# Kernel tuning notes

Measured on AMD Instinct MI355X. Metric: run time of the kernel, lower is better.

Reference implementation:

```python
import jax, jax.numpy as jnp
import numpy as np

N = 50000      # num nodes
E = 800000     # num edges
F_IN = 128     # CONFIG.FeatureLen()
H = 100        # conv1_hide
C = 16         # CONFIG.ClassNum()
LEAKY = 0.01


def setup_inputs() -> dict:
    key = jax.random.key(0)
    k = jax.random.split(key, 4)
    x = jax.random.normal(k[0], (N, F_IN), dtype=jnp.float32)
    edge_index = jax.random.randint(k[1], (2, E), 0, N, dtype=jnp.int32)
    W1 = jax.random.normal(k[2], (F_IN, H), dtype=jnp.float32) / np.sqrt(F_IN).astype(np.float32)
    b1 = jnp.zeros((H,), dtype=jnp.float32)
    W2 = jax.random.normal(k[3], (H, C), dtype=jnp.float32) / np.sqrt(H).astype(np.float32)
    b2 = jnp.zeros((C,), dtype=jnp.float32)
    return {"x": x, "W1": W1, "b1": b1, "W2": W2, "b2": b2, "edge_index": edge_index}


def _gcn_conv(x, W, b, src, dst):
    """PyG GCNConv: x' = D^{-1/2}(A+I)D^{-1/2} X W + b (symmetric norm, self-loops)."""
    x = x @ W  # transform first (smaller feature dim for propagation)
    loop = jnp.arange(N, dtype=src.dtype)
    s = jnp.concatenate([src, loop])  # sources (message senders)
    d = jnp.concatenate([dst, loop])  # targets (message receivers)
    deg = jax.ops.segment_sum(jnp.ones_like(d, dtype=x.dtype), d, num_segments=N)
    dinv = jnp.where(deg > 0, jax.lax.rsqrt(deg), 0.0)
    norm = dinv[s] * dinv[d]                      # [E+N]
    msg = x[s] * norm[:, None]                    # gather + scale
    out = jax.ops.segment_sum(msg, d, num_segments=N)  # scatter-add
    return out + b


def reference(x, W1, b1, W2, b2, edge_index):
    src, dst = edge_index[0], edge_index[1]
    h = _gcn_conv(x, W1, b1, src, dst)
    h = jax.nn.leaky_relu(h, negative_slope=LEAKY)
    # dropout is identity in eval mode (training=False)
    h = _gcn_conv(h, W2, b2, src, dst)
    return jax.nn.log_softmax(h, axis=1)
```

## Files before the change

### kernel.cpp

```cpp
#include <hip/hip_runtime.h>

#define F_IN 128
#define HDIM 100
#define HPAD 128
#define CDIM 16
#define CAP  64
#define BT_STRIDE 136
#define CHUNK 4096
#define KMAX 200
#define RCAP 64

static constexpr float LEAKY = 0.01f;

using short8  = __attribute__((ext_vector_type(8))) short;
using float4v = __attribute__((ext_vector_type(4))) float;
using float2v = __attribute__((ext_vector_type(2))) float;

__device__ __forceinline__ unsigned short f2bf(float f) {
    unsigned u = __float_as_uint(f);
    u += 0x7fffu + ((u >> 16) & 1u);
    return (unsigned short)(u >> 16);
}


__global__ __launch_bounds__(256) void k_gemm1_p1(const float* __restrict__ x,
                                                  const float* __restrict__ W1,
                                                  unsigned char* __restrict__ y1f8,
                                                  const int* __restrict__ src,
                                                  const int* __restrict__ dst,
                                                  unsigned* __restrict__ bkt_edges,
                                                  int* __restrict__ cnt_arr,
                                                  int N, int E, int FB, int KBKT, int GB) {
    __shared__ union {
        unsigned short bt[F_IN * BT_STRIDE];
        struct { unsigned stage[CHUNK]; int cnt[KMAX]; } p1;
    } sm;
    int bx = blockIdx.x;
    int t = threadIdx.x;

    if (bx < FB) {
        unsigned* stage = sm.p1.stage;
        int* cnt = sm.p1.cnt;
        for (int i = t; i < KBKT; i += 256) cnt[i] = 0;
        __syncthreads();
        int e0 = bx * CHUNK, e1 = min(E, e0 + CHUNK);
        for (int i = e0 + t; i < e1; i += 256) {
            int d = dst[i];
            unsigned pk = ((unsigned)d << 16) | (unsigned)src[i];
            atomicAdd(&cnt[d >> 8], 1);
            stage[i - e0] = pk;
        }
        __syncthreads();
        for (int i = t; i < KBKT; i += 256) cnt_arr[bx * KBKT + i] = cnt[i];
        __syncthreads();
        for (int i = t; i < KBKT; i += 256) cnt[i] = 0;
        __syncthreads();
        int m = e1 - e0;
        for (int i = t; i < m; i += 256) {
            unsigned pk = stage[i];
            int b = pk >> 24;
            int pos = atomicAdd(&cnt[b], 1);
            if (pos < RCAP)
                bkt_edges[((size_t)b * FB + bx) * RCAP + pos] = pk;
        }
        return;
    }

    for (int idx = t; idx < F_IN * HPAD; idx += 256) {
        int k = idx >> 7;
        int n = idx & 127;
        float v = (n < HDIM) ? W1[k * HDIM + n] : 0.f;
        sm.bt[n * BT_STRIDE + k] = f2bf(v);
    }
    __syncthreads();

    int wave = t >> 6, lane = t & 63;
    int Mtiles = (N + 15) >> 4;
    int m = lane & 15;
    int kq = lane >> 4;

    for (int tile = (bx - FB) * 4 + wave; tile < Mtiles; tile += 4 * GB) {
        int row0 = tile * 16;
        int arow = min(row0 + m, N - 1);
        const float* xrow = x + (size_t)arow * F_IN;

        short8 afrag[4];
        #pragma unroll
        for (int kt = 0; kt < 4; ++kt) {
            int kb = kt * 32 + kq * 8;
            float4 a0 = *(const float4*)(xrow + kb);
            float4 a1 = *(const float4*)(xrow + kb + 4);
            short8 f;
            f[0] = (short)f2bf(a0.x); f[1] = (short)f2bf(a0.y);
            f[2] = (short)f2bf(a0.z); f[3] = (short)f2bf(a0.w);
            f[4] = (short)f2bf(a1.x); f[5] = (short)f2bf(a1.y);
            f[6] = (short)f2bf(a1.z); f[7] = (short)f2bf(a1.w);
            afrag[kt] = f;
        }

        bool full = (row0 + 15 < N);
        #pragma unroll
        for (int ct = 0; ct < 8; ++ct) {
            float4v acc = {0.f, 0.f, 0.f, 0.f};
            #pragma unroll
            for (int kt = 0; kt < 4; ++kt) {
                short8 b = *(const short8*)&sm.bt[(ct * 16 + m) * BT_STRIDE + kt * 32 + kq * 8];
                acc = __builtin_amdgcn_mfma_f32_16x16x32_bf16(afrag[kt], b, acc, 0, 0, 0);
            }
            #pragma unroll
            for (int i = 0; i < 4; ++i) {
                int r = row0 + kq * 4 + i;
                int v8 = __builtin_amdgcn_cvt_pk_fp8_f32(acc[i], acc[i], 0, false);
                if (full || r < N)
                    y1f8[(size_t)r * HPAD + ct * 16 + m] = (unsigned char)(v8 & 0xff);
            }
        }
    }
}


__global__ __launch_bounds__(256) void k_p2(const unsigned* __restrict__ bkt_edges,
                                            const int* __restrict__ cnt_arr,
                                            int* __restrict__ deg,
                                            unsigned short* __restrict__ slots,
                                            int N, int FB, int KBKT) {
    __shared__ int cur[256];
    int b = blockIdx.x, t = threadIdx.x;
    cur[t] = 0;
    __syncthreads();
    for (int fb = t; fb < FB; fb += 256) {
        int c = cnt_arr[fb * KBKT + b];
        size_t base = ((size_t)b * FB + fb) * RCAP;
        for (int j = 0; j < c; ++j) {
            unsigned pk = bkt_edges[base + j];
            int d = pk >> 16;
            int pos = atomicAdd(&cur[d & 255], 1);
            if (pos < CAP)
                slots[(size_t)d * CAP + pos] = (unsigned short)(pk & 0xffffu);
        }
    }
    __syncthreads();
    int n = (b << 8) + t;
    if (n < N) deg[n] = cur[t];
}


__global__ __launch_bounds__(256) void k_agg1y2(const unsigned* __restrict__ y1u,
                                                const float* __restrict__ b1,
                                                const float* __restrict__ W2,
                                                const int* __restrict__ deg,
                                                const unsigned short* __restrict__ slots,
                                                float* __restrict__ y2, int N) {
    __shared__ float W2s[HDIM * CDIM];
    __shared__ float hs[4][2][HPAD];
    int t = threadIdx.x;
    for (int idx = t; idx < HDIM * CDIM; idx += 256) W2s[idx] = W2[idx];
    __syncthreads();

    int wave = t >> 6, lane = t & 63;
    int half = lane >> 5, l = lane & 31;
    int hbase = lane & 32;
    int n = blockIdx.x * 8 + wave * 2 + half;
    bool valid = (n < N);
    int nn = valid ? n : (N - 1);

    int beg = nn * CAP;
    int cnt = valid ? deg[nn] : 0;
    float dn = rsqrtf((float)deg[nn] + 1.0f);

    int cother = __shfl(cnt, lane ^ 32);
    int cmax = max(cnt, cother);

    float a0 = 0.f, a1 = 0.f, a2 = 0.f, a3 = 0.f;
    for (int e0 = 0; e0 < cmax; e0 += 32) {
        int mm = min(32, cnt - e0);
        unsigned su = 0u; float wv = 0.f;
        if (l < mm) {
            su = slots[beg + e0 + l];
            wv = rsqrtf((float)deg[su] + 1.0f);
        }
        int mmax = min(32, cmax - e0);
        int mpad = (mmax + 7) & ~7;
        for (int j = 0; j < mpad; j += 8) {
            float w[8]; unsigned vv[8];
            #pragma unroll
            for (int q = 0; q < 8; ++q) {
                int ln = hbase | (j + q);
                unsigned s = (unsigned)__shfl((int)su, ln);
                w[q] = __shfl(wv, ln);
                vv[q] = y1u[(size_t)s * 32 + l];
            }
            #pragma unroll
            for (int q = 0; q < 8; ++q) {
                float2v lov = __builtin_amdgcn_cvt_pk_f32_fp8((int)vv[q], false);
                float2v hiv = __builtin_amdgcn_cvt_pk_f32_fp8((int)vv[q], true);
                a0 = fmaf(w[q], lov[0], a0);
                a1 = fmaf(w[q], lov[1], a1);
                a2 = fmaf(w[q], hiv[0], a2);
                a3 = fmaf(w[q], hiv[1], a3);
            }
        }
    }
    {
        unsigned vn = y1u[(size_t)nn * 32 + l];
        float2v lov = __builtin_amdgcn_cvt_pk_f32_fp8((int)vn, false);
        float2v hiv = __builtin_amdgcn_cvt_pk_f32_fp8((int)vn, true);
        a0 = fmaf(dn, lov[0], a0);
        a1 = fmaf(dn, lov[1], a1);
        a2 = fmaf(dn, hiv[0], a2);
        a3 = fmaf(dn, hiv[1], a3);
    }

    float4 bb = (l < 25) ? *(const float4*)&b1[4 * l] : make_float4(0.f, 0.f, 0.f, 0.f);
    float h0 = fmaf(dn, a0, bb.x);
    float h1 = fmaf(dn, a1, bb.y);
    float h2 = fmaf(dn, a2, bb.z);
    float h3 = fmaf(dn, a3, bb.w);
    h0 = h0 > 0.f ? h0 : LEAKY * h0;
    h1 = h1 > 0.f ? h1 : LEAKY * h1;
    h2 = h2 > 0.f ? h2 : LEAKY * h2;
    h3 = h3 > 0.f ? h3 : LEAKY * h3;
    *(float4*)&hs[wave][half][4 * l] = make_float4(h0, h1, h2, h3);
    __builtin_amdgcn_wave_barrier();

    int c = l & 15, kg = l >> 4;
    const float* hrow = hs[wave][half];
    float p = 0.f;
    #pragma unroll 10
    for (int j = 0; j < 50; ++j) {
        int k = 2 * j + kg;
        p = fmaf(hrow[k], W2s[k * CDIM + c], p);
    }
    p += __shfl_down(p, 16);
    if (l < 16 && valid) y2[(size_t)n * CDIM + c] = p;
}


__global__ __launch_bounds__(256) void k_agg2(const float* __restrict__ y2,
                                              const float* __restrict__ b2,
                                              const int* __restrict__ deg,
                                              const unsigned short* __restrict__ slots,
                                              float* __restrict__ out, int N) {
    int t = threadIdx.x;
    int wave = t >> 6, lane = t & 63;
    int sub = lane >> 4, c = lane & 15;
    int n = blockIdx.x * 16 + wave * 4 + sub;
    bool valid = (n < N);
    int nn = valid ? n : 0;

    int beg = nn * CAP;
    int cnt = valid ? deg[nn] : 0;
    float dn = rsqrtf((float)deg[nn] + 1.0f);
    float acc = dn * y2[(size_t)nn * CDIM + c];

    for (int e0 = 0; e0 < cnt; e0 += 16) {
        int mm = min(16, cnt - e0);
        unsigned su = 0u; float wv = 0.f;
        if (c < mm) {
            su = slots[beg + e0 + c];
            wv = rsqrtf((float)deg[su] + 1.0f);
        }
        int mpad = (mm + 3) & ~3;
        for (int j = 0; j < mpad; j += 4) {
            float w[4]; float v[4];
            #pragma unroll
            for (int q = 0; q < 4; ++q) {
                int ln = sub * 16 + j + q;
                unsigned s = (unsigned)__shfl((int)su, ln);
                w[q] = __shfl(wv, ln);
                v[q] = y2[(size_t)s * CDIM + c];
            }
            #pragma unroll
            for (int q = 0; q < 4; ++q) acc = fmaf(w[q], v[q], acc);
        }
    }

    float lg = fmaf(dn, acc, b2[c]);
    float mx = lg;
    #pragma unroll
    for (int k = 8; k; k >>= 1) mx = fmaxf(mx, __shfl_xor(mx, k));
    float ex = __expf(lg - mx);
    #pragma unroll
    for (int k = 8; k; k >>= 1) ex += __shfl_xor(ex, k);
    float lse = mx + __logf(ex);
    if (valid) out[(size_t)n * CDIM + c] = lg - lse;
}


extern "C" void kernel_launch(void* const* d_in, const int* in_sizes, int n_in,
                              void* d_out, int out_size, void* d_ws, size_t ws_size,
                              hipStream_t stream) {
    const float* x  = (const float*)d_in[0];
    const float* W1 = (const float*)d_in[1];
    const float* b1 = (const float*)d_in[2];
    const float* W2 = (const float*)d_in[3];
    const float* b2 = (const float*)d_in[4];
    const int*   ei = (const int*)d_in[5];

    const int N = in_sizes[0] / F_IN;
    const int E = in_sizes[5] / 2;
    const int* src = ei;
    const int* dst = ei + E;

    const int KBKT = (N + 255) >> 8;
    const int FB   = (E + CHUNK - 1) / CHUNK;

    char* ws = (char*)d_ws;
    size_t off = 0;
    auto alloc = [&](size_t bytes) {
        char* p = ws + off;
        off += (bytes + 255) & ~(size_t)255;
        return p;
    };
    int*            deg       = (int*)alloc((size_t)N * 4);
    unsigned char*  y1f8      = (unsigned char*)alloc((size_t)N * HPAD);
    float*          y2        = (float*)alloc((size_t)N * CDIM * 4);
    unsigned short* slots     = (unsigned short*)alloc((size_t)N * CAP * 2);
    int*            cnt_arr   = (int*)alloc((size_t)FB * KBKT * 4);
    unsigned*       bkt_edges = (unsigned*)alloc((size_t)KBKT * FB * RCAP * 4);
    (void)ws_size; (void)n_in; (void)out_size;

    const int GB = 262;

    k_gemm1_p1<<<FB + GB, 256, 0, stream>>>(x, W1, y1f8, src, dst,
                                            bkt_edges, cnt_arr, N, E, FB, KBKT, GB);
    k_p2<<<KBKT, 256, 0, stream>>>(bkt_edges, cnt_arr, deg, slots, N, FB, KBKT);
    k_agg1y2<<<(N + 7) / 8, 256, 0, stream>>>((const unsigned*)y1f8, b1, W2,
                                              deg, slots, y2, N);
    k_agg2<<<(N + 15) / 16, 256, 0, stream>>>(y2, b2, deg, slots,
                                              (float*)d_out, N);
}
```

Before: 163.3 us.

## Replace two-pass bucketed CSR build with direct global atomic scatter

Removes the block-local bucketing pass and the separate k_p2 kernel. Edges are now scattered straight into per-node slot lists using global atomicAdd on deg, after a memset. This drops the intermediate bucket buffers and one kernel launch, but relies on many scattered global atomics and makes slot order nondeterministic.

```diff
diff --git a/kernel.cpp b/kernel.cpp
--- a/kernel.cpp
+++ b/kernel.cpp
@@ -6,9 +6,6 @@
 #define CDIM 16
 #define CAP  64
 #define BT_STRIDE 136
-#define CHUNK 4096
-#define KMAX 200
-#define RCAP 64
 
 static constexpr float LEAKY = 0.01f;
 
@@ -23,45 +20,26 @@
 }
 
 
-__global__ __launch_bounds__(256) void k_gemm1_p1(const float* __restrict__ x,
-                                                  const float* __restrict__ W1,
-                                                  unsigned char* __restrict__ y1f8,
-                                                  const int* __restrict__ src,
-                                                  const int* __restrict__ dst,
-                                                  unsigned* __restrict__ bkt_edges,
-                                                  int* __restrict__ cnt_arr,
-                                                  int N, int E, int FB, int KBKT, int GB) {
-    __shared__ union {
-        unsigned short bt[F_IN * BT_STRIDE];
-        struct { unsigned stage[CHUNK]; int cnt[KMAX]; } p1;
-    } sm;
+__global__ __launch_bounds__(256) void k_gemm1_scat(const float* __restrict__ x,
+                                                    const float* __restrict__ W1,
+                                                    unsigned char* __restrict__ y1f8,
+                                                    const int* __restrict__ src,
+                                                    const int* __restrict__ dst,
+                                                    int* __restrict__ deg,
+                                                    unsigned short* __restrict__ slots,
+                                                    int N, int E, int GB, int SC) {
+    __shared__ unsigned short bt[F_IN * BT_STRIDE];
     int bx = blockIdx.x;
     int t = threadIdx.x;
 
-    if (bx < FB) {
-        unsigned* stage = sm.p1.stage;
-        int* cnt = sm.p1.cnt;
-        for (int i = t; i < KBKT; i += 256) cnt[i] = 0;
-        __syncthreads();
-        int e0 = bx * CHUNK, e1 = min(E, e0 + CHUNK);
-        for (int i = e0 + t; i < e1; i += 256) {
+    if (bx >= GB) {
+        int stride = SC * 256;
+        for (int i = (bx - GB) * 256 + t; i < E; i += stride) {
             int d = dst[i];
-            unsigned pk = ((unsigned)d << 16) | (unsigned)src[i];
-            atomicAdd(&cnt[d >> 8], 1);
-            stage[i - e0] = pk;
-        }
-        __syncthreads();
-        for (int i = t; i < KBKT; i += 256) cnt_arr[bx * KBKT + i] = cnt[i];
-        __syncthreads();
-        for (int i = t; i < KBKT; i += 256) cnt[i] = 0;
-        __syncthreads();
-        int m = e1 - e0;
-        for (int i = t; i < m; i += 256) {
-            unsigned pk = stage[i];
-            int b = pk >> 24;
-            int pos = atomicAdd(&cnt[b], 1);
-            if (pos < RCAP)
-                bkt_edges[((size_t)b * FB + bx) * RCAP + pos] = pk;
+            int s = src[i];
+            int pos = atomicAdd(&deg[d], 1);
+            if (pos < CAP)
+                slots[(size_t)d * CAP + pos] = (unsigned short)s;
         }
         return;
     }
@@ -70,7 +48,7 @@
         int k = idx >> 7;
         int n = idx & 127;
         float v = (n < HDIM) ? W1[k * HDIM + n] : 0.f;
-        sm.bt[n * BT_STRIDE + k] = f2bf(v);
+        bt[n * BT_STRIDE + k] = f2bf(v);
     }
     __syncthreads();
 
@@ -79,7 +57,7 @@
     int m = lane & 15;
     int kq = lane >> 4;
 
-    for (int tile = (bx - FB) * 4 + wave; tile < Mtiles; tile += 4 * GB) {
+    for (int tile = bx * 4 + wave; tile < Mtiles; tile += 4 * GB) {
         int row0 = tile * 16;
         int arow = min(row0 + m, N - 1);
         const float* xrow = x + (size_t)arow * F_IN;
@@ -104,7 +82,7 @@
             float4v acc = {0.f, 0.f, 0.f, 0.f};
             #pragma unroll
             for (int kt = 0; kt < 4; ++kt) {
-                short8 b = *(const short8*)&sm.bt[(ct * 16 + m) * BT_STRIDE + kt * 32 + kq * 8];
+                short8 b = *(const short8*)&bt[(ct * 16 + m) * BT_STRIDE + kt * 32 + kq * 8];
                 acc = __builtin_amdgcn_mfma_f32_16x16x32_bf16(afrag[kt], b, acc, 0, 0, 0);
             }
             #pragma unroll
@@ -116,32 +94,6 @@
             }
         }
     }
-}
-
-
-__global__ __launch_bounds__(256) void k_p2(const unsigned* __restrict__ bkt_edges,
-                                            const int* __restrict__ cnt_arr,
-                                            int* __restrict__ deg,
-                                            unsigned short* __restrict__ slots,
-                                            int N, int FB, int KBKT) {
-    __shared__ int cur[256];
-    int b = blockIdx.x, t = threadIdx.x;
-    cur[t] = 0;
-    __syncthreads();
-    for (int fb = t; fb < FB; fb += 256) {
-        int c = cnt_arr[fb * KBKT + b];
-        size_t base = ((size_t)b * FB + fb) * RCAP;
-        for (int j = 0; j < c; ++j) {
-            unsigned pk = bkt_edges[base + j];
-            int d = pk >> 16;
-            int pos = atomicAdd(&cur[d & 255], 1);
-            if (pos < CAP)
-                slots[(size_t)d * CAP + pos] = (unsigned short)(pk & 0xffffu);
-        }
-    }
-    __syncthreads();
-    int n = (b << 8) + t;
-    if (n < N) deg[n] = cur[t];
 }
 
 
@@ -302,9 +254,6 @@
     const int* src = ei;
     const int* dst = ei + E;
 
-    const int KBKT = (N + 255) >> 8;
-    const int FB   = (E + CHUNK - 1) / CHUNK;
-
     char* ws = (char*)d_ws;
     size_t off = 0;
     auto alloc = [&](size_t bytes) {
@@ -312,19 +261,18 @@
         off += (bytes + 255) & ~(size_t)255;
         return p;
     };
-    int*            deg       = (int*)alloc((size_t)N * 4);
-    unsigned char*  y1f8      = (unsigned char*)alloc((size_t)N * HPAD);
-    float*          y2        = (float*)alloc((size_t)N * CDIM * 4);
-    unsigned short* slots     = (unsigned short*)alloc((size_t)N * CAP * 2);
-    int*            cnt_arr   = (int*)alloc((size_t)FB * KBKT * 4);
-    unsigned*       bkt_edges = (unsigned*)alloc((size_t)KBKT * FB * RCAP * 4);
+    int*            deg   = (int*)alloc((size_t)N * 4);
+    unsigned char*  y1f8  = (unsigned char*)alloc((size_t)N * HPAD);
+    float*          y2    = (float*)alloc((size_t)N * CDIM * 4);
+    unsigned short* slots = (unsigned short*)alloc((size_t)N * CAP * 2);
     (void)ws_size; (void)n_in; (void)out_size;
 
     const int GB = 262;
-
-    k_gemm1_p1<<<FB + GB, 256, 0, stream>>>(x, W1, y1f8, src, dst,
-                                            bkt_edges, cnt_arr, N, E, FB, KBKT, GB);
-    k_p2<<<KBKT, 256, 0, stream>>>(bkt_edges, cnt_arr, deg, slots, N, FB, KBKT);
+    const int SC = 512;
+
+    hipMemsetAsync(deg, 0, (size_t)N * 4, stream);
+    k_gemm1_scat<<<GB + SC, 256, 0, stream>>>(x, W1, y1f8, src, dst,
+                                              deg, slots, N, E, GB, SC);
     k_agg1y2<<<(N + 7) / 8, 256, 0, stream>>>((const unsigned*)y1f8, b1, W2,
                                               deg, slots, y2, N);
     k_agg2<<<(N + 15) / 16, 256, 0, stream>>>(y2, b2, deg, slots,
```

Result: slower. 171.5 us (+5.1%).

## Replace layer-2 pull aggregation with atomic edge push and precomputed dinv

Applied to the files above, without the earlier changes.

Degree normalisation factors are computed once in the bucketing kernel and stored, so the aggregation kernels no longer recompute rsqrt per neighbour. The second-layer aggregation becomes two kernels. The first pushes pre-scaled y2 rows along the raw edge list with float atomics into an accumulator seeded with the self-loop term, and a separate kernel applies the destination scale, the bias and log-softmax. This drops the per-node slot walk and shuffles in exchange for 12.8M global atomics, an extra kernel launch, and non-deterministic summation order.

```diff
diff --git a/kernel.cpp b/kernel.cpp
--- a/kernel.cpp
+++ b/kernel.cpp
@@ -122,6 +122,7 @@
 __global__ __launch_bounds__(256) void k_p2(const unsigned* __restrict__ bkt_edges,
                                             const int* __restrict__ cnt_arr,
                                             int* __restrict__ deg,
+                                            float* __restrict__ dinv,
                                             unsigned short* __restrict__ slots,
                                             int N, int FB, int KBKT) {
     __shared__ int cur[256];
@@ -141,7 +142,10 @@
     }
     __syncthreads();
     int n = (b << 8) + t;
-    if (n < N) deg[n] = cur[t];
+    if (n < N) {
+        deg[n] = cur[t];
+        dinv[n] = rsqrtf((float)cur[t] + 1.0f);
+    }
 }
 
 
@@ -149,8 +153,11 @@
                                                 const float* __restrict__ b1,
                                                 const float* __restrict__ W2,
                                                 const int* __restrict__ deg,
+                                                const float* __restrict__ dinv,
                                                 const unsigned short* __restrict__ slots,
-                                                float* __restrict__ y2, int N) {
+                                                float* __restrict__ y2s,
+                                                float* __restrict__ acc,
+                                                int N) {
     __shared__ float W2s[HDIM * CDIM];
     __shared__ float hs[4][2][HPAD];
     int t = threadIdx.x;
@@ -166,7 +173,7 @@
 
     int beg = nn * CAP;
     int cnt = valid ? deg[nn] : 0;
-    float dn = rsqrtf((float)deg[nn] + 1.0f);
+    float dn = dinv[nn];
 
     int cother = __shfl(cnt, lane ^ 32);
     int cmax = max(cnt, cother);
@@ -177,7 +184,7 @@
         unsigned su = 0u; float wv = 0.f;
         if (l < mm) {
             su = slots[beg + e0 + l];
-            wv = rsqrtf((float)deg[su] + 1.0f);
+            wv = dinv[su];
         }
         int mmax = min(32, cmax - e0);
         int mpad = (mmax + 7) & ~7;
@@ -232,15 +239,34 @@
         p = fmaf(hrow[k], W2s[k * CDIM + c], p);
     }
     p += __shfl_down(p, 16);
-    if (l < 16 && valid) y2[(size_t)n * CDIM + c] = p;
-}
-
-
-__global__ __launch_bounds__(256) void k_agg2(const float* __restrict__ y2,
-                                              const float* __restrict__ b2,
-                                              const int* __restrict__ deg,
-                                              const unsigned short* __restrict__ slots,
-                                              float* __restrict__ out, int N) {
+    if (l < 16 && valid) {
+        float v = dn * p;
+        y2s[(size_t)n * CDIM + c] = v;
+        acc[(size_t)n * CDIM + c] = v;
+    }
+}
+
+
+__global__ __launch_bounds__(256) void k_push2(const float* __restrict__ y2s,
+                                               const int* __restrict__ src,
+                                               const int* __restrict__ dst,
+                                               float* __restrict__ acc,
+                                               int E, int NGRP) {
+    int c = threadIdx.x & 15;
+    int g = (blockIdx.x * 256 + threadIdx.x) >> 4;
+    for (int e = g; e < E; e += NGRP) {
+        int s = src[e];
+        int d = dst[e];
+        float v = y2s[(size_t)s * CDIM + c];
+        atomicAdd(&acc[(size_t)d * CDIM + c], v);
+    }
+}
+
+
+__global__ __launch_bounds__(256) void k_lsm(const float* __restrict__ acc,
+                                             const float* __restrict__ dinv,
+                                             const float* __restrict__ b2,
+                                             float* __restrict__ out, int N) {
     int t = threadIdx.x;
     int wave = t >> 6, lane = t & 63;
     int sub = lane >> 4, c = lane & 15;
@@ -248,34 +274,7 @@
     bool valid = (n < N);
     int nn = valid ? n : 0;
 
-    int beg = nn * CAP;
-    int cnt = valid ? deg[nn] : 0;
-    float dn = rsqrtf((float)deg[nn] + 1.0f);
-    float acc = dn * y2[(size_t)nn * CDIM + c];
-
-    for (int e0 = 0; e0 < cnt; e0 += 16) {
-        int mm = min(16, cnt - e0);
-        unsigned su = 0u; float wv = 0.f;
-        if (c < mm) {
-            su = slots[beg + e0 + c];
-            wv = rsqrtf((float)deg[su] + 1.0f);
-        }
-        int mpad = (mm + 3) & ~3;
-        for (int j = 0; j < mpad; j += 4) {
-            float w[4]; float v[4];
-            #pragma unroll
-            for (int q = 0; q < 4; ++q) {
-                int ln = sub * 16 + j + q;
-                unsigned s = (unsigned)__shfl((int)su, ln);
-                w[q] = __shfl(wv, ln);
-                v[q] = y2[(size_t)s * CDIM + c];
-            }
-            #pragma unroll
-            for (int q = 0; q < 4; ++q) acc = fmaf(w[q], v[q], acc);
-        }
-    }
-
-    float lg = fmaf(dn, acc, b2[c]);
+    float lg = fmaf(dinv[nn], acc[(size_t)nn * CDIM + c], b2[c]);
     float mx = lg;
     #pragma unroll
     for (int k = 8; k; k >>= 1) mx = fmaxf(mx, __shfl_xor(mx, k));
@@ -313,20 +312,24 @@
         return p;
     };
     int*            deg       = (int*)alloc((size_t)N * 4);
+    float*          dinv      = (float*)alloc((size_t)N * 4);
     unsigned char*  y1f8      = (unsigned char*)alloc((size_t)N * HPAD);
-    float*          y2        = (float*)alloc((size_t)N * CDIM * 4);
+    float*          y2s       = (float*)alloc((size_t)N * CDIM * 4);
+    float*          acc       = (float*)alloc((size_t)N * CDIM * 4);
     unsigned short* slots     = (unsigned short*)alloc((size_t)N * CAP * 2);
     int*            cnt_arr   = (int*)alloc((size_t)FB * KBKT * 4);
     unsigned*       bkt_edges = (unsigned*)alloc((size_t)KBKT * FB * RCAP * 4);
     (void)ws_size; (void)n_in; (void)out_size;
 
     const int GB = 262;
+    const int PB = 2048;
+    const int NGRP = PB * 256 / 16;
 
     k_gemm1_p1<<<FB + GB, 256, 0, stream>>>(x, W1, y1f8, src, dst,
                                             bkt_edges, cnt_arr, N, E, FB, KBKT, GB);
-    k_p2<<<KBKT, 256, 0, stream>>>(bkt_edges, cnt_arr, deg, slots, N, FB, KBKT);
+    k_p2<<<KBKT, 256, 0, stream>>>(bkt_edges, cnt_arr, deg, dinv, slots, N, FB, KBKT);
     k_agg1y2<<<(N + 7) / 8, 256, 0, stream>>>((const unsigned*)y1f8, b1, W2,
-                                              deg, slots, y2, N);
-    k_agg2<<<(N + 15) / 16, 256, 0, stream>>>(y2, b2, deg, slots,
-                                              (float*)d_out, N);
-}
+                                              deg, dinv, slots, y2s, acc, N);
+    k_push2<<<PB, 256, 0, stream>>>(y2s, src, dst, acc, E, NGRP);
+    k_lsm<<<(N + 15) / 16, 256, 0, stream>>>(acc, dinv, b2, (float*)d_out, N);
+}
```

Result: slower. 195.0 us (+19.5%).
